# Kernel optimization log

Measured on AMD Instinct MI355X. Metric: run time of the kernel, lower is better.

Reference implementation:

```python
import jax, jax.numpy as jnp
import numpy as np

NEG_SLOPE = 0.01  # torch nn.LeakyReLU default


def setup_inputs() -> dict:
    key = jax.random.key(0)
    k1, k2, k3, k4, k5 = jax.random.split(key, 5)
    N, K, S, H = 50000, 32, 128, 4
    x = jax.random.normal(k1, (N, S), dtype=jnp.float32)          # node sentence vectors
    neighbors = jax.random.randint(k2, (N, K), 0, N)              # padded neighbor ids
    mask = jax.random.uniform(k3, (N, K)) < 0.75                  # valid-neighbor mask
    # DQA.B_ij per head: Linear(2*S -> 1), init std=0.05
    W = jax.random.normal(k4, (H, 2 * S), dtype=jnp.float32) * 0.05
    b = jax.random.normal(k5, (H,), dtype=jnp.float32) * 0.05
    return {"x": x, "W": W, "b": b, "neighbors": neighbors,
            "mask": mask, "propagate_count": 2}


def _leaky_relu(v):
    return jnp.where(v >= 0, v, NEG_SLOPE * v)


def reference(x, W, b, neighbors, mask, propagate_count):
    # x: [N,S]; W: [H,2S]; b: [H]; neighbors: [N,K] int; mask: [N,K] bool
    S = x.shape[-1]
    wa, wb = W[:, :S], W[:, S:]  # score = wa.x_center + wb.x_row + b

    def step(h):
        sa = h @ wa.T                                  # [N,H] center contribution
        sb = h @ wb.T                                  # [N,H] row contribution
        s_self = _leaky_relu(sa + sb + b)              # [N,H]   row 0 (self)
        s_nbr = _leaky_relu(sa[:, None, :] + sb[neighbors] + b)  # [N,K,H]
        s_nbr = jnp.where(mask[:, :, None], s_nbr, -jnp.inf)
        s_all = jnp.concatenate([s_self[:, None, :], s_nbr], axis=1)  # [N,K+1,H]
        p = jax.nn.softmax(s_all, axis=1)              # softmax over rows
        xg = h[neighbors]                              # [N,K,S] gather
        # weighted sum of rows, per head
        out = p[:, 0, :, None] * h[:, None, :] \
              + jnp.einsum('nkh,nks->nhs', p[:, 1:, :], xg)  # [N,H,S]
        # D_attention: sum over heads / n_heads, then ReLU
        return jax.nn.relu(out.mean(axis=1))           # [N,S]

    for _ in range(int(propagate_count)):
        x = step(x)
    return x
```

## Files before the change

### kernel.cpp

```cpp
#include <hip/hip_runtime.h>
#include <math.h>

#define S_DIM   128
#define K_NB    32
#define H_HEADS 4
#define WL_STRIDE 288
#define NSLOT   36

#if defined(__has_builtin)
#  if __has_builtin(__builtin_amdgcn_permlane16_swap)
#    define HAVE_PL16 1
#  endif
#  if __has_builtin(__builtin_amdgcn_permlane32_swap)
#    define HAVE_PL32 1
#  endif
#  if __has_builtin(__builtin_elementwise_fma)
#    define HAVE_EFMA 1
#  endif
#  if __has_builtin(__builtin_elementwise_max)
#    define HAVE_EMAX 1
#  endif
#endif

typedef float f32x2 __attribute__((ext_vector_type(2)));

__device__ __forceinline__ f32x2 pkfma(f32x2 a, f32x2 b, f32x2 c) {
#ifdef HAVE_EFMA
    return __builtin_elementwise_fma(a, b, c);
#else
    return a * b + c;
#endif
}
__device__ __forceinline__ f32x2 pkrelu(f32x2 a) {
#ifdef HAVE_EMAX
    return __builtin_elementwise_max(a, (f32x2){0.f, 0.f});
#else
    f32x2 r; r.x = fmaxf(a.x, 0.f); r.y = fmaxf(a.y, 0.f); return r;
#endif
}

__device__ __forceinline__ float lrelu(float v) { return fmaxf(v, 0.01f * v); }

template <int CTRL>
__device__ __forceinline__ float dpp_add(float x) {
    const int v = __builtin_amdgcn_update_dpp(0, __float_as_int(x), CTRL, 0xF, 0xF, true);
    return x + __int_as_float(v);
}
__device__ __forceinline__ float rowsum16(float x) {
    x = dpp_add<0xB1>(x);
    x = dpp_add<0x4E>(x);
    x = dpp_add<0x141>(x);
    x = dpp_add<0x140>(x);
    return x;
}

__device__ __forceinline__ float bfly_add16(float x) {
#ifdef HAVE_PL16
    auto r = __builtin_amdgcn_permlane16_swap(__float_as_uint(x), __float_as_uint(x), false, false);
    return __uint_as_float(r[0]) + __uint_as_float(r[1]);
#else
    return x + __shfl_xor(x, 16, 64);
#endif
}
__device__ __forceinline__ float bfly_add32(float x) {
#ifdef HAVE_PL32
    auto r = __builtin_amdgcn_permlane32_swap(__float_as_uint(x), __float_as_uint(x), false, false);
    return __uint_as_float(r[0]) + __uint_as_float(r[1]);
#else
    return x + __shfl_xor(x, 32, 64);
#endif
}

__device__ __forceinline__ unsigned bf16rne(float f) {
    unsigned u = __float_as_uint(f);
    return (u + 0x7fffu + ((u >> 16) & 1u)) >> 16;
}
__device__ __forceinline__ unsigned pack2(float lo, float hi) {
    return bf16rne(lo) | (bf16rne(hi) << 16);
}
__device__ __forceinline__ f32x2 up2(unsigned u) {
    f32x2 r;
    r.x = __uint_as_float(u << 16);
    r.y = __uint_as_float(u & 0xffff0000u);
    return r;
}

__global__ __launch_bounds__(256) void proj_kernel(const float* __restrict__ h,
                                                   const float* __restrict__ W,
                                                   float* __restrict__ sasb,
                                                   unsigned* __restrict__ hb_out,
                                                   const unsigned int* __restrict__ maskw,
                                                   int* __restrict__ flag, int N) {
    __shared__ float Wl[H_HEADS * 2 * S_DIM];
    for (int i = threadIdx.x; i < 1024; i += 256) Wl[i] = W[i];

    if (blockIdx.x == 0) {
        __shared__ int nb, nf;
        if (threadIdx.x == 0) { nb = 0; nf = 0; }
        __syncthreads();
        bool bin = true, f32 = true;
        for (int i = threadIdx.x; i < 2048; i += 256) {
            unsigned v = maskw[i];
            if (v > 1u) bin = false;
            if (v != 0u && v != 0x3F800000u) f32 = false;
        }
        if (!bin) atomicOr(&nb, 1);
        if (!f32) atomicOr(&nf, 1);
        __syncthreads();
        if (threadIdx.x == 0) *flag = nb ? (nf ? 2 : 1) : 0;
    }
    __syncthreads();

    const int wv = threadIdx.x >> 6;
    const int lane = threadIdx.x & 63;
    const int half = lane >> 5;
    const int hl = lane & 31;
    const int n = blockIdx.x * 8 + wv * 2 + half;
    if (n >= N) return;

    const float4 hv = reinterpret_cast<const float4*>(h)[(size_t)n * 32 + hl];
    {
        uint2 hb2;
        hb2.x = pack2(hv.x, hv.y);
        hb2.y = pack2(hv.z, hv.w);
        reinterpret_cast<uint2*>(hb_out)[(size_t)n * 32 + hl] = hb2;
    }

    const int c = 4 * hl;
    float p[8];
#pragma unroll
    for (int i = 0; i < 4; ++i) {
        const float4 wa = *reinterpret_cast<const float4*>(&Wl[i * 256 + c]);
        const float4 wb = *reinterpret_cast<const float4*>(&Wl[i * 256 + 128 + c]);
        p[i]     = hv.x * wa.x + hv.y * wa.y + hv.z * wa.z + hv.w * wa.w;
        p[i + 4] = hv.x * wb.x + hv.y * wb.y + hv.z * wb.z + hv.w * wb.w;
    }

    float a[8];
#pragma unroll
    for (int i = 0; i < 8; ++i) a[i] = bfly_add16(p[i]);
    const bool qlo = hl < 16;
    float r0 = qlo ? a[0] : a[4], r1 = qlo ? a[1] : a[5];
    float r2 = qlo ? a[2] : a[6], r3 = qlo ? a[3] : a[7];
    r0 = rowsum16(r0); r1 = rowsum16(r1);
    r2 = rowsum16(r2); r3 = rowsum16(r3);
    if (hl == 0)
        *reinterpret_cast<float4*>(sasb + (size_t)n * 8) = make_float4(r0, r1, r2, r3);
    if (hl == 16)
        *reinterpret_cast<float4*>(sasb + (size_t)n * 8 + 4) = make_float4(r0, r1, r2, r3);
}

__global__ __launch_bounds__(256) void attn_kernel(const uint4* __restrict__ hb,
                                                   const float* __restrict__ sasb,
                                                   const float* __restrict__ bvec,
                                                   const int* __restrict__ nbr,
                                                   const void* __restrict__ mask,
                                                   const int* __restrict__ maskmode,
                                                   float* __restrict__ fout,
                                                   uint4* __restrict__ hb_out,
                                                   float* __restrict__ sasb_next,
                                                   const float* __restrict__ W, int N) {
    __shared__ float2 qr_sh[4][NSLOT];
    __shared__ float Wl[H_HEADS * WL_STRIDE];

    if (sasb_next) {
        for (int i = threadIdx.x; i < 1024; i += 256) {
            const int hh = i >> 8, c = i & 255;
            Wl[hh * WL_STRIDE + c + (c >> 3)] = W[i];
        }
        __syncthreads();
    }

    const int wv = threadIdx.x >> 6;
    const int lane = threadIdx.x & 63;
    const int n = blockIdx.x * 4 + wv;
    if (n >= N) return;
    const int mode = *maskmode;

    const float b0 = bvec[0], b1 = bvec[1], b2 = bvec[2], b3 = bvec[3];
    const float4 sa = *reinterpret_cast<const float4*>(sasb + (size_t)n * 8);
    const float4 sbs = *reinterpret_cast<const float4*>(sasb + (size_t)n * 8 + 4);
    const float es0 = __expf(lrelu(sa.x + sbs.x + b0));
    const float es1 = __expf(lrelu(sa.y + sbs.y + b1));
    const float es2 = __expf(lrelu(sa.z + sbs.z + b2));
    const float es3 = __expf(lrelu(sa.w + sbs.w + b3));

    float l0 = -INFINITY, l1 = -INFINITY, l2 = -INFINITY, l3 = -INFINITY;
    int row = 0;
    bool valid = false;
    if (lane < K_NB) {
        row = nbr[(size_t)n * K_NB + lane];
        if (mode == 0)
            valid = reinterpret_cast<const int*>(mask)[(size_t)n * K_NB + lane] != 0;
        else if (mode == 1)
            valid = reinterpret_cast<const float*>(mask)[(size_t)n * K_NB + lane] != 0.f;
        else
            valid = reinterpret_cast<const unsigned char*>(mask)[(size_t)n * K_NB + lane] != 0;
    }
    if (valid) {
        const float4 sbr = *reinterpret_cast<const float4*>(sasb + (size_t)row * 8 + 4);
        l0 = lrelu(sa.x + sbr.x + b0);
        l1 = lrelu(sa.y + sbr.y + b1);
        l2 = lrelu(sa.z + sbr.z + b2);
        l3 = lrelu(sa.w + sbr.w + b3);
    }

    const float e0 = __expf(l0);
    const float e1 = __expf(l1);
    const float e2 = __expf(l2);
    const float e3 = __expf(l3);

    float s0 = rowsum16(e0), s1 = rowsum16(e1);
    float s2 = rowsum16(e2), s3 = rowsum16(e3);
    s0 = bfly_add16(s0); s1 = bfly_add16(s1);
    s2 = bfly_add16(s2); s3 = bfly_add16(s3);
    s0 += es0; s1 += es1; s2 += es2; s3 += es3;
    const float i0 = __builtin_amdgcn_rcpf(s0);
    const float i1 = __builtin_amdgcn_rcpf(s1);
    const float i2 = __builtin_amdgcn_rcpf(s2);
    const float i3 = __builtin_amdgcn_rcpf(s3);

    const unsigned long long bm = __ballot(valid);
    const int nv1 = __popcll(bm) + 1;
    {
        const int ps = nv1 + lane;
        if (ps < NSLOT) qr_sh[wv][ps] = make_float2(0.f, __int_as_float(n));
    }
    if (valid) {
        const int pos = 1 + __popcll(bm & ((1ull << lane) - 1ull));
        qr_sh[wv][pos] = make_float2(
            0.25f * (e0 * i0 + e1 * i1 + e2 * i2 + e3 * i3), __int_as_float(row));
    }
    if (lane == 0)
        qr_sh[wv][0] = make_float2(
            0.25f * (es0 * i0 + es1 * i1 + es2 * i2 + es3 * i3), __int_as_float(n));

    const int grp = lane >> 4;
    const int sl = lane & 15;

    float2 qr[9];
#pragma unroll
    for (int t = 0; t < 9; ++t) qr[t] = qr_sh[wv][grp + 4 * t];

    uint4 v[9];
#pragma unroll
    for (int t = 0; t < 9; ++t) {
        const unsigned idx = ((unsigned)__float_as_int(qr[t].y) << 4) + (unsigned)sl;
        v[t] = hb[idx];
    }

    f32x2 acc2[4];
#pragma unroll
    for (int p = 0; p < 4; ++p) acc2[p] = (f32x2){0.f, 0.f};
#pragma unroll
    for (int t = 0; t < 9; ++t) {
        const float q = qr[t].x;
        const f32x2 q2 = {q, q};
        acc2[0] = pkfma(q2, up2(v[t].x), acc2[0]);
        acc2[1] = pkfma(q2, up2(v[t].y), acc2[1]);
        acc2[2] = pkfma(q2, up2(v[t].z), acc2[2]);
        acc2[3] = pkfma(q2, up2(v[t].w), acc2[3]);
    }

#pragma unroll
    for (int p = 0; p < 4; ++p) {
        acc2[p].x = bfly_add16(acc2[p].x);
        acc2[p].y = bfly_add16(acc2[p].y);
        acc2[p].x = bfly_add32(acc2[p].x);
        acc2[p].y = bfly_add32(acc2[p].y);
        acc2[p] = pkrelu(acc2[p]);
    }

    if (lane < 32) {
        const int g1 = grp & 1;
        const f32x2 lo2 = g1 ? acc2[2] : acc2[0];
        const f32x2 hi2 = g1 ? acc2[3] : acc2[1];
        if (hb_out) {
            uint2 o;
            o.x = pack2(lo2.x, lo2.y);
            o.y = pack2(hi2.x, hi2.y);
            reinterpret_cast<uint2*>(hb_out)[(size_t)n * 32 + sl * 2 + g1] = o;
        }
        if (fout) {
            reinterpret_cast<float4*>(fout)[(size_t)n * 32 + sl * 2 + g1] =
                make_float4(lo2.x, lo2.y, hi2.x, hi2.y);
        }
    }

    if (sasb_next) {
        const int base = (lane >> 5) ? 128 : 0;
        const int boff = base + (base >> 3) + sl * 9;
        f32x2 rp0 = {0.f, 0.f}, rp1 = {0.f, 0.f}, rp2 = {0.f, 0.f}, rp3 = {0.f, 0.f};
#pragma unroll
        for (int p = 0; p < 4; ++p) {
            const f32x2 a2 = acc2[p];
            const int j = boff + 2 * p;
            rp0 = pkfma(a2, (f32x2){Wl[0 * WL_STRIDE + j], Wl[0 * WL_STRIDE + j + 1]}, rp0);
            rp1 = pkfma(a2, (f32x2){Wl[1 * WL_STRIDE + j], Wl[1 * WL_STRIDE + j + 1]}, rp1);
            rp2 = pkfma(a2, (f32x2){Wl[2 * WL_STRIDE + j], Wl[2 * WL_STRIDE + j + 1]}, rp2);
            rp3 = pkfma(a2, (f32x2){Wl[3 * WL_STRIDE + j], Wl[3 * WL_STRIDE + j + 1]}, rp3);
        }
        float r0 = rowsum16(rp0.x + rp0.y);
        float r1 = rowsum16(rp1.x + rp1.y);
        float r2 = rowsum16(rp2.x + rp2.y);
        float r3 = rowsum16(rp3.x + rp3.y);
        if (lane == 0)
            *reinterpret_cast<float4*>(sasb_next + (size_t)n * 8) = make_float4(r0, r1, r2, r3);
        if (lane == 32)
            *reinterpret_cast<float4*>(sasb_next + (size_t)n * 8 + 4) = make_float4(r0, r1, r2, r3);
    }
}


extern "C" void kernel_launch(void* const* d_in, const int* in_sizes, int n_in,
                              void* d_out, int out_size, void* d_ws, size_t ws_size,
                              hipStream_t stream) {
    const float* x = (const float*)d_in[0];
    const float* W = (const float*)d_in[1];
    const float* b = (const float*)d_in[2];
    const int* nbr = (const int*)d_in[3];
    const void* mask = d_in[4];

    const int N = in_sizes[0] / S_DIM;

    char* ws = (char*)d_ws;
    float* sasb = (float*)ws;
    size_t off = (size_t)N * 8 * sizeof(float);
    off = (off + 255) & ~(size_t)255;
    int* flag = (int*)(ws + off);
    off += 256;
    float* sasb2 = (float*)(ws + off);
    off += (size_t)N * 8 * sizeof(float);
    off = (off + 255) & ~(size_t)255;
    unsigned* xb = (unsigned*)(ws + off);
    off += (size_t)N * S_DIM * 2;
    uint4* h1b = (uint4*)(ws + off);

    float* out = (float*)d_out;
    const int ablocks = (N + 3) / 4;
    const int pblocks = (N + 7) / 8;

    proj_kernel<<<pblocks, 256, 0, stream>>>(x, W, sasb, xb, (const unsigned int*)mask, flag, N);
    attn_kernel<<<ablocks, 256, 0, stream>>>((const uint4*)xb, sasb, b, nbr, mask, flag,
                                             nullptr, h1b, sasb2, W, N);
    attn_kernel<<<ablocks, 256, 0, stream>>>(h1b, sasb2, b, nbr, mask, flag,
                                             out, nullptr, nullptr, W, N);
}
```

Measured before the change: 115.6 us.

## Split attention into score and channel-chunked gather kernels over transposed bf16 features

The fused attention kernel is replaced by three pieces. A qrow kernel computes per-neighbor softmax weights and stores each as fp16 packed with a 16-bit row index. A gather kernel then works on one 32-channel chunk at a time, reading from a chunk-major transposed bf16 feature layout. The point is to shrink the working set of the random neighbor gathers so they hit in cache more often. In exchange there are more launches, extra global traffic for the packed weight/index table, and projT recomputes the second-layer projection from bf16 instead of fusing it. The packing also only works when N fits in 16 bits and lowers weight precision to fp16.

Measured after the change: 162.1 us. +40.3%, slower.

```diff
diff --git a/kernel.cpp b/kernel.cpp
--- a/kernel.cpp
+++ b/kernel.cpp
@@ -1,11 +1,12 @@
 #include <hip/hip_runtime.h>
+#include <hip/hip_fp16.h>
 #include <math.h>
 
 #define S_DIM   128
 #define K_NB    32
 #define H_HEADS 4
-#define WL_STRIDE 288
 #define NSLOT   36
+#define NCHUNK  4
 
 #if defined(__has_builtin)
 #  if __has_builtin(__builtin_amdgcn_permlane16_swap)
@@ -84,11 +85,14 @@
     r.y = __uint_as_float(u & 0xffff0000u);
     return r;
 }
+__device__ __forceinline__ float qdec(unsigned u) {
+    return __half2float(__ushort_as_half((unsigned short)(u & 0xffffu)));
+}
 
 __global__ __launch_bounds__(256) void proj_kernel(const float* __restrict__ h,
                                                    const float* __restrict__ W,
                                                    float* __restrict__ sasb,
-                                                   unsigned* __restrict__ hb_out,
+                                                   uint2* __restrict__ xbT,
                                                    const unsigned int* __restrict__ maskw,
                                                    int* __restrict__ flag, int N) {
     __shared__ float Wl[H_HEADS * 2 * S_DIM];
@@ -98,14 +102,14 @@
         __shared__ int nb, nf;
         if (threadIdx.x == 0) { nb = 0; nf = 0; }
         __syncthreads();
-        bool bin = true, f32 = true;
+        bool bin = true, f32ok = true;
         for (int i = threadIdx.x; i < 2048; i += 256) {
             unsigned v = maskw[i];
             if (v > 1u) bin = false;
-            if (v != 0u && v != 0x3F800000u) f32 = false;
+            if (v != 0u && v != 0x3F800000u) f32ok = false;
         }
         if (!bin) atomicOr(&nb, 1);
-        if (!f32) atomicOr(&nf, 1);
+        if (!f32ok) atomicOr(&nf, 1);
         __syncthreads();
         if (threadIdx.x == 0) *flag = nb ? (nf ? 2 : 1) : 0;
     }
@@ -119,23 +123,23 @@
     if (n >= N) return;
 
     const float4 hv = reinterpret_cast<const float4*>(h)[(size_t)n * 32 + hl];
-    {
-        uint2 hb2;
-        hb2.x = pack2(hv.x, hv.y);
-        hb2.y = pack2(hv.z, hv.w);
-        reinterpret_cast<uint2*>(hb_out)[(size_t)n * 32 + hl] = hb2;
-    }
-
-    const int c = 4 * hl;
+    if (xbT) {
+        const int c = hl >> 3, s = hl & 7;
+        uint2 o;
+        o.x = pack2(hv.x, hv.y);
+        o.y = pack2(hv.z, hv.w);
+        xbT[((size_t)c * N + n) * 8 + s] = o;
+    }
+
+    const int c4 = 4 * hl;
     float p[8];
 #pragma unroll
     for (int i = 0; i < 4; ++i) {
-        const float4 wa = *reinterpret_cast<const float4*>(&Wl[i * 256 + c]);
-        const float4 wb = *reinterpret_cast<const float4*>(&Wl[i * 256 + 128 + c]);
+        const float4 wa = *reinterpret_cast<const float4*>(&Wl[i * 256 + c4]);
+        const float4 wb = *reinterpret_cast<const float4*>(&Wl[i * 256 + 128 + c4]);
         p[i]     = hv.x * wa.x + hv.y * wa.y + hv.z * wa.z + hv.w * wa.w;
         p[i + 4] = hv.x * wb.x + hv.y * wb.y + hv.z * wb.z + hv.w * wb.w;
     }
-
     float a[8];
 #pragma unroll
     for (int i = 0; i < 8; ++i) a[i] = bfly_add16(p[i]);
@@ -150,27 +154,55 @@
         *reinterpret_cast<float4*>(sasb + (size_t)n * 8 + 4) = make_float4(r0, r1, r2, r3);
 }
 
-__global__ __launch_bounds__(256) void attn_kernel(const uint4* __restrict__ hb,
-                                                   const float* __restrict__ sasb,
+__global__ __launch_bounds__(256) void projT_kernel(const uint2* __restrict__ hbT,
+                                                    const float* __restrict__ W,
+                                                    float* __restrict__ sasb, int N) {
+    __shared__ float Wl[H_HEADS * 2 * S_DIM];
+    for (int i = threadIdx.x; i < 1024; i += 256) Wl[i] = W[i];
+    __syncthreads();
+
+    const int wv = threadIdx.x >> 6;
+    const int lane = threadIdx.x & 63;
+    const int half = lane >> 5;
+    const int hl = lane & 31;
+    const int n = blockIdx.x * 8 + wv * 2 + half;
+    if (n >= N) return;
+
+    const int c = hl >> 3, s = hl & 7;
+    const uint2 w = hbT[((size_t)c * N + n) * 8 + s];
+    const f32x2 d0 = up2(w.x);
+    const f32x2 d1 = up2(w.y);
+    const float4 hv = make_float4(d0.x, d0.y, d1.x, d1.y);
+
+    const int c4 = 4 * hl;
+    float p[8];
+#pragma unroll
+    for (int i = 0; i < 4; ++i) {
+        const float4 wa = *reinterpret_cast<const float4*>(&Wl[i * 256 + c4]);
+        const float4 wb = *reinterpret_cast<const float4*>(&Wl[i * 256 + 128 + c4]);
+        p[i]     = hv.x * wa.x + hv.y * wa.y + hv.z * wa.z + hv.w * wa.w;
+        p[i + 4] = hv.x * wb.x + hv.y * wb.y + hv.z * wb.z + hv.w * wb.w;
+    }
+    float a[8];
+#pragma unroll
+    for (int i = 0; i < 8; ++i) a[i] = bfly_add16(p[i]);
+    const bool qlo = hl < 16;
+    float r0 = qlo ? a[0] : a[4], r1 = qlo ? a[1] : a[5];
+    float r2 = qlo ? a[2] : a[6], r3 = qlo ? a[3] : a[7];
+    r0 = rowsum16(r0); r1 = rowsum16(r1);
+    r2 = rowsum16(r2); r3 = rowsum16(r3);
+    if (hl == 0)
+        *reinterpret_cast<float4*>(sasb + (size_t)n * 8) = make_float4(r0, r1, r2, r3);
+    if (hl == 16)
+        *reinterpret_cast<float4*>(sasb + (size_t)n * 8 + 4) = make_float4(r0, r1, r2, r3);
+}
+
+__global__ __launch_bounds__(256) void qrow_kernel(const float* __restrict__ sasb,
                                                    const float* __restrict__ bvec,
                                                    const int* __restrict__ nbr,
                                                    const void* __restrict__ mask,
                                                    const int* __restrict__ maskmode,
-                                                   float* __restrict__ fout,
-                                                   uint4* __restrict__ hb_out,
-                                                   float* __restrict__ sasb_next,
-                                                   const float* __restrict__ W, int N) {
-    __shared__ float2 qr_sh[4][NSLOT];
-    __shared__ float Wl[H_HEADS * WL_STRIDE];
-
-    if (sasb_next) {
-        for (int i = threadIdx.x; i < 1024; i += 256) {
-            const int hh = i >> 8, c = i & 255;
-            Wl[hh * WL_STRIDE + c + (c >> 3)] = W[i];
-        }
-        __syncthreads();
-    }
-
+                                                   unsigned* __restrict__ qrow, int N) {
     const int wv = threadIdx.x >> 6;
     const int lane = threadIdx.x & 63;
     const int n = blockIdx.x * 4 + wv;
@@ -186,7 +218,7 @@
     const float es3 = __expf(lrelu(sa.w + sbs.w + b3));
 
     float l0 = -INFINITY, l1 = -INFINITY, l2 = -INFINITY, l3 = -INFINITY;
-    int row = 0;
+    int row = n;
     bool valid = false;
     if (lane < K_NB) {
         row = nbr[(size_t)n * K_NB + lane];
@@ -214,100 +246,125 @@
     float s2 = rowsum16(e2), s3 = rowsum16(e3);
     s0 = bfly_add16(s0); s1 = bfly_add16(s1);
     s2 = bfly_add16(s2); s3 = bfly_add16(s3);
+    s0 = bfly_add32(s0); s1 = bfly_add32(s1);
+    s2 = bfly_add32(s2); s3 = bfly_add32(s3);
     s0 += es0; s1 += es1; s2 += es2; s3 += es3;
     const float i0 = __builtin_amdgcn_rcpf(s0);
     const float i1 = __builtin_amdgcn_rcpf(s1);
     const float i2 = __builtin_amdgcn_rcpf(s2);
     const float i3 = __builtin_amdgcn_rcpf(s3);
 
-    const unsigned long long bm = __ballot(valid);
-    const int nv1 = __popcll(bm) + 1;
-    {
-        const int ps = nv1 + lane;
-        if (ps < NSLOT) qr_sh[wv][ps] = make_float2(0.f, __int_as_float(n));
-    }
-    if (valid) {
-        const int pos = 1 + __popcll(bm & ((1ull << lane) - 1ull));
-        qr_sh[wv][pos] = make_float2(
-            0.25f * (e0 * i0 + e1 * i1 + e2 * i2 + e3 * i3), __int_as_float(row));
-    }
-    if (lane == 0)
-        qr_sh[wv][0] = make_float2(
-            0.25f * (es0 * i0 + es1 * i1 + es2 * i2 + es3 * i3), __int_as_float(n));
-
-    const int grp = lane >> 4;
-    const int sl = lane & 15;
-
-    float2 qr[9];
-#pragma unroll
-    for (int t = 0; t < 9; ++t) qr[t] = qr_sh[wv][grp + 4 * t];
-
-    uint4 v[9];
-#pragma unroll
-    for (int t = 0; t < 9; ++t) {
-        const unsigned idx = ((unsigned)__float_as_int(qr[t].y) << 4) + (unsigned)sl;
-        v[t] = hb[idx];
-    }
+    if (lane < NSLOT) {
+        float q;
+        unsigned rs;
+        if (lane < K_NB) {
+            q = valid ? 0.25f * (e0 * i0 + e1 * i1 + e2 * i2 + e3 * i3) : 0.f;
+            rs = valid ? (unsigned)row : (unsigned)n;
+        } else if (lane == K_NB) {
+            q = 0.25f * (es0 * i0 + es1 * i1 + es2 * i2 + es3 * i3);
+            rs = (unsigned)n;
+        } else {
+            q = 0.f;
+            rs = (unsigned)n;
+        }
+        const unsigned qb = (unsigned)__half_as_ushort(__float2half_rn(q));
+        qrow[(size_t)n * NSLOT + lane] = (rs << 16) | qb;
+    }
+}
+
+template <int BF16SRC>
+__global__ __launch_bounds__(256) void gather_kernel(const void* __restrict__ src_,
+                                                     const unsigned* __restrict__ qrow,
+                                                     uint4* __restrict__ hbT_out,
+                                                     float* __restrict__ fout, int N) {
+    const int wv = threadIdx.x >> 6;
+    const int lane = threadIdx.x & 63;
+    const int b = blockIdx.x;
+    const int c = (b & 7) >> 1;
+    const int n = (b >> 3) * 8 + (b & 1) * 4 + wv;
+    if (n >= N) return;
+
+    const int sub = lane >> 4;
+    const int sg = lane & 15;
+
+    const unsigned base = (unsigned)n * NSLOT;
+    const unsigned u0 = qrow[base + sg];
+    const unsigned u1 = qrow[base + 16 + sg];
+    unsigned u2 = 0u;
+    if (sg < 4) u2 = qrow[base + 32 + sg];
+    const unsigned r0 = u0 >> 16, r1 = u1 >> 16, r2 = u2 >> 16;
+    const float q0 = qdec(u0), q1 = qdec(u1), q2 = qdec(u2);
 
     f32x2 acc2[4];
 #pragma unroll
     for (int p = 0; p < 4; ++p) acc2[p] = (f32x2){0.f, 0.f};
-#pragma unroll
-    for (int t = 0; t < 9; ++t) {
-        const float q = qr[t].x;
-        const f32x2 q2 = {q, q};
-        acc2[0] = pkfma(q2, up2(v[t].x), acc2[0]);
-        acc2[1] = pkfma(q2, up2(v[t].y), acc2[1]);
-        acc2[2] = pkfma(q2, up2(v[t].z), acc2[2]);
-        acc2[3] = pkfma(q2, up2(v[t].w), acc2[3]);
+
+    if (BF16SRC) {
+        const uint4* __restrict__ src = (const uint4*)src_;
+        const unsigned cb = (unsigned)c * (unsigned)N;
+        const uint4 v0 = src[(size_t)(cb + r0) * 4 + sub];
+        const uint4 v1 = src[(size_t)(cb + r1) * 4 + sub];
+        const uint4 v2 = src[(size_t)(cb + r2) * 4 + sub];
+        const f32x2 qa = {q0, q0}, qb = {q1, q1}, qc = {q2, q2};
+        acc2[0] = pkfma(qa, up2(v0.x), acc2[0]);
+        acc2[1] = pkfma(qa, up2(v0.y), acc2[1]);
+        acc2[2] = pkfma(qa, up2(v0.z), acc2[2]);
+        acc2[3] = pkfma(qa, up2(v0.w), acc2[3]);
+        acc2[0] = pkfma(qb, up2(v1.x), acc2[0]);
+        acc2[1] = pkfma(qb, up2(v1.y), acc2[1]);
+        acc2[2] = pkfma(qb, up2(v1.z), acc2[2]);
+        acc2[3] = pkfma(qb, up2(v1.w), acc2[3]);
+        acc2[0] = pkfma(qc, up2(v2.x), acc2[0]);
+        acc2[1] = pkfma(qc, up2(v2.y), acc2[1]);
+        acc2[2] = pkfma(qc, up2(v2.z), acc2[2]);
+        acc2[3] = pkfma(qc, up2(v2.w), acc2[3]);
+    } else {
+        const float* __restrict__ src = (const float*)src_;
+        const unsigned off = (unsigned)c * 32 + (unsigned)sub * 8;
+        const float4 a0 = *reinterpret_cast<const float4*>(src + (size_t)r0 * 128 + off);
+        const float4 a1 = *reinterpret_cast<const float4*>(src + (size_t)r0 * 128 + off + 4);
+        const float4 b0 = *reinterpret_cast<const float4*>(src + (size_t)r1 * 128 + off);
+        const float4 b1 = *reinterpret_cast<const float4*>(src + (size_t)r1 * 128 + off + 4);
+        const float4 c0 = *reinterpret_cast<const float4*>(src + (size_t)r2 * 128 + off);
+        const float4 c1 = *reinterpret_cast<const float4*>(src + (size_t)r2 * 128 + off + 4);
+        const f32x2 qa = {q0, q0}, qb = {q1, q1}, qc = {q2, q2};
+        acc2[0] = pkfma(qa, (f32x2){a0.x, a0.y}, acc2[0]);
+        acc2[1] = pkfma(qa, (f32x2){a0.z, a0.w}, acc2[1]);
+        acc2[2] = pkfma(qa, (f32x2){a1.x, a1.y}, acc2[2]);
+        acc2[3] = pkfma(qa, (f32x2){a1.z, a1.w}, acc2[3]);
+        acc2[0] = pkfma(qb, (f32x2){b0.x, b0.y}, acc2[0]);
+        acc2[1] = pkfma(qb, (f32x2){b0.z, b0.w}, acc2[1]);
+        acc2[2] = pkfma(qb, (f32x2){b1.x, b1.y}, acc2[2]);
+        acc2[3] = pkfma(qb, (f32x2){b1.z, b1.w}, acc2[3]);
+        acc2[0] = pkfma(qc, (f32x2){c0.x, c0.y}, acc2[0]);
+        acc2[1] = pkfma(qc, (f32x2){c0.z, c0.w}, acc2[1]);
+        acc2[2] = pkfma(qc, (f32x2){c1.x, c1.y}, acc2[2]);
+        acc2[3] = pkfma(qc, (f32x2){c1.z, c1.w}, acc2[3]);
     }
 
 #pragma unroll
     for (int p = 0; p < 4; ++p) {
-        acc2[p].x = bfly_add16(acc2[p].x);
-        acc2[p].y = bfly_add16(acc2[p].y);
-        acc2[p].x = bfly_add32(acc2[p].x);
-        acc2[p].y = bfly_add32(acc2[p].y);
+        acc2[p].x = rowsum16(acc2[p].x);
+        acc2[p].y = rowsum16(acc2[p].y);
         acc2[p] = pkrelu(acc2[p]);
     }
 
-    if (lane < 32) {
-        const int g1 = grp & 1;
-        const f32x2 lo2 = g1 ? acc2[2] : acc2[0];
-        const f32x2 hi2 = g1 ? acc2[3] : acc2[1];
-        if (hb_out) {
-            uint2 o;
-            o.x = pack2(lo2.x, lo2.y);
-            o.y = pack2(hi2.x, hi2.y);
-            reinterpret_cast<uint2*>(hb_out)[(size_t)n * 32 + sl * 2 + g1] = o;
-        }
-        if (fout) {
-            reinterpret_cast<float4*>(fout)[(size_t)n * 32 + sl * 2 + g1] =
-                make_float4(lo2.x, lo2.y, hi2.x, hi2.y);
-        }
-    }
-
-    if (sasb_next) {
-        const int base = (lane >> 5) ? 128 : 0;
-        const int boff = base + (base >> 3) + sl * 9;
-        f32x2 rp0 = {0.f, 0.f}, rp1 = {0.f, 0.f}, rp2 = {0.f, 0.f}, rp3 = {0.f, 0.f};
-#pragma unroll
-        for (int p = 0; p < 4; ++p) {
-            const f32x2 a2 = acc2[p];
-            const int j = boff + 2 * p;
-            rp0 = pkfma(a2, (f32x2){Wl[0 * WL_STRIDE + j], Wl[0 * WL_STRIDE + j + 1]}, rp0);
-            rp1 = pkfma(a2, (f32x2){Wl[1 * WL_STRIDE + j], Wl[1 * WL_STRIDE + j + 1]}, rp1);
-            rp2 = pkfma(a2, (f32x2){Wl[2 * WL_STRIDE + j], Wl[2 * WL_STRIDE + j + 1]}, rp2);
-            rp3 = pkfma(a2, (f32x2){Wl[3 * WL_STRIDE + j], Wl[3 * WL_STRIDE + j + 1]}, rp3);
-        }
-        float r0 = rowsum16(rp0.x + rp0.y);
-        float r1 = rowsum16(rp1.x + rp1.y);
-        float r2 = rowsum16(rp2.x + rp2.y);
-        float r3 = rowsum16(rp3.x + rp3.y);
-        if (lane == 0)
-            *reinterpret_cast<float4*>(sasb_next + (size_t)n * 8) = make_float4(r0, r1, r2, r3);
-        if (lane == 32)
-            *reinterpret_cast<float4*>(sasb_next + (size_t)n * 8 + 4) = make_float4(r0, r1, r2, r3);
+    if (hbT_out && sg == 0) {
+        uint4 o;
+        o.x = pack2(acc2[0].x, acc2[0].y);
+        o.y = pack2(acc2[1].x, acc2[1].y);
+        o.z = pack2(acc2[2].x, acc2[2].y);
+        o.w = pack2(acc2[3].x, acc2[3].y);
+        hbT_out[((size_t)c * N + n) * 4 + sub] = o;
+    }
+    if (fout) {
+        float* dst = fout + (size_t)n * 128 + c * 32 + sub * 8;
+        if (sg == 0)
+            *reinterpret_cast<float4*>(dst) =
+                make_float4(acc2[0].x, acc2[0].y, acc2[1].x, acc2[1].y);
+        if (sg == 8)
+            *reinterpret_cast<float4*>(dst + 4) =
+                make_float4(acc2[2].x, acc2[2].y, acc2[3].x, acc2[3].y);
     }
 }
 
@@ -324,25 +381,31 @@
     const int N = in_sizes[0] / S_DIM;
 
     char* ws = (char*)d_ws;
-    float* sasb = (float*)ws;
-    size_t off = (size_t)N * 8 * sizeof(float);
-    off = (off + 255) & ~(size_t)255;
+    size_t off = 0;
+    unsigned* qrow = (unsigned*)(ws + off);
+    off += ((size_t)N * NSLOT * 4 + 255) & ~(size_t)255;
+    float* sasb = (float*)(ws + off);
+    off += ((size_t)N * 8 * 4 + 255) & ~(size_t)255;
     int* flag = (int*)(ws + off);
     off += 256;
-    float* sasb2 = (float*)(ws + off);
-    off += (size_t)N * 8 * sizeof(float);
-    off = (off + 255) & ~(size_t)255;
-    unsigned* xb = (unsigned*)(ws + off);
-    off += (size_t)N * S_DIM * 2;
-    uint4* h1b = (uint4*)(ws + off);
+    uint4* h1bT = (uint4*)(ws + off);
+    off += (size_t)NCHUNK * N * 64;
+    uint2* xbT = (uint2*)(ws + off);
+    const bool use_xbT = (off + (size_t)NCHUNK * N * 64) <= ws_size;
 
     float* out = (float*)d_out;
+    const int pblocks = (N + 7) / 8;
     const int ablocks = (N + 3) / 4;
-    const int pblocks = (N + 7) / 8;
-
-    proj_kernel<<<pblocks, 256, 0, stream>>>(x, W, sasb, xb, (const unsigned int*)mask, flag, N);
-    attn_kernel<<<ablocks, 256, 0, stream>>>((const uint4*)xb, sasb, b, nbr, mask, flag,
-                                             nullptr, h1b, sasb2, W, N);
-    attn_kernel<<<ablocks, 256, 0, stream>>>(h1b, sasb2, b, nbr, mask, flag,
-                                             out, nullptr, nullptr, W, N);
-}
+    const int bblocks = ((N + 7) / 8) * 8;
+
+    proj_kernel<<<pblocks, 256, 0, stream>>>(x, W, sasb, use_xbT ? xbT : nullptr,
+                                             (const unsigned int*)mask, flag, N);
+    qrow_kernel<<<ablocks, 256, 0, stream>>>(sasb, b, nbr, mask, flag, qrow, N);
+    if (use_xbT)
+        gather_kernel<1><<<bblocks, 256, 0, stream>>>((const void*)xbT, qrow, h1bT, nullptr, N);
+    else
+        gather_kernel<0><<<bblocks, 256, 0, stream>>>((const void*)x, qrow, h1bT, nullptr, N);
+    projT_kernel<<<pblocks, 256, 0, stream>>>((const uint2*)h1bT, W, sasb, N);
+    qrow_kernel<<<ablocks, 256, 0, stream>>>(sasb, b, nbr, mask, flag, qrow, N);
+    gather_kernel<1><<<bblocks, 256, 0, stream>>>((const void*)h1bT, qrow, nullptr, out, N);
+}
```
